# Performance work log

Measured on AMD Instinct MI355X. Metric: run time of the kernel, lower is better.

Reference implementation:

```python
import jax, jax.numpy as jnp
import numpy as np

D_MODEL = 3072
N_HEADS = 24
HEAD_DIM = D_MODEL // N_HEADS          # 128
Q_PROJ = D_MODEL // 2                  # 1536
KV_PROJ = 2 * D_MODEL // 3             # 2048
ROPE_DIM = HEAD_DIM // 2               # 64 (qk_rope_dim == qk_no_rope_dim)
MAX_LEN = 2048
ROPE_THETA = 10000.0
EPS = 1e-6
B, S = 2, 2048


def setup_inputs() -> dict:
    key = jax.random.key(0)
    ks = jax.random.split(key, 7)
    return {
        "x": jax.random.normal(ks[0], (B, S, D_MODEL), dtype=jnp.float32),
        "scale": jnp.ones((D_MODEL,), dtype=jnp.float32),
        "w_dq": 0.01 * jax.random.normal(ks[1], (D_MODEL, Q_PROJ), dtype=jnp.float32),
        "w_uq": 0.01 * jax.random.normal(ks[2], (Q_PROJ, D_MODEL), dtype=jnp.float32),
        "w_dkv": 0.01 * jax.random.normal(ks[3], (D_MODEL, KV_PROJ + ROPE_DIM), dtype=jnp.float32),
        "w_ukv": 0.01 * jax.random.normal(ks[4], (KV_PROJ, D_MODEL + N_HEADS * ROPE_DIM), dtype=jnp.float32),
        "w_o": 0.01 * jax.random.normal(ks[5], (D_MODEL, D_MODEL), dtype=jnp.float32),
    }


def _rope_cos_sin(seq_len):
    # freqs over full head_dim, sliced to rope_dim//2 then tiled x2 (as in torch repeat)
    freqs = 1.0 / (ROPE_THETA ** (jnp.arange(0, HEAD_DIM, 2, dtype=jnp.float32) / HEAD_DIM))
    angles = jnp.arange(seq_len, dtype=jnp.float32)[:, None] * freqs[None, :]  # [S, 64]
    ang = angles[:, : ROPE_DIM // 2]                                            # [S, 32]
    cos = jnp.tile(jnp.cos(ang), (1, 2))                                        # [S, 64]
    sin = jnp.tile(jnp.sin(ang), (1, 2))
    return cos[None, None], sin[None, None]  # [1,1,S,64]


def _rotate_half(t):
    a, b = jnp.split(t, 2, axis=-1)
    return jnp.concatenate([-b, a], axis=-1)


def reference(x, scale, w_dq, w_uq, w_dkv, w_ukv, w_o):
    b, s, _ = x.shape
    # RMSNorm pre-normalization
    xn = scale * (x * jax.lax.rsqrt(jnp.mean(x * x, axis=-1, keepdims=True) + EPS))
    # two-stage query projection
    q = (xn @ w_dq) @ w_uq                                   # [B,S,D]
    q = q.reshape(b, s, N_HEADS, HEAD_DIM).transpose(0, 2, 1, 3)  # [B,H,S,hd]
    q_no_rope, q_rope = jnp.split(q, [ROPE_DIM], axis=-1)
    cos, sin = _rope_cos_sin(s)
    q_rope = q_rope * cos + _rotate_half(q_rope) * sin
    # KV down projection (this is the kv cache)
    kv_down = xn @ w_dkv                                     # [B,S,KV_PROJ+rope]
    kv_no_rope, k_rope = jnp.split(kv_down, [KV_PROJ], axis=-1)
    # KV up projection
    kv_up = kv_no_rope @ w_ukv                               # [B,S,H*(hd+rope)]
    kv_up = kv_up.reshape(b, s, N_HEADS, HEAD_DIM + ROPE_DIM).transpose(0, 2, 1, 3)
    key, value = jnp.split(kv_up, [ROPE_DIM], axis=-1)       # key [B,H,S,64], value [B,H,S,128]
    # shared rope key (one head, broadcast to all heads)
    k_rope = k_rope[:, None, :, :]                           # [B,1,S,64]
    k_rope = k_rope * cos + _rotate_half(k_rope) * sin
    k_rope = jnp.broadcast_to(k_rope, (b, N_HEADS, s, ROPE_DIM))
    final_q = jnp.concatenate([q_no_rope, q_rope], axis=-1)  # [B,H,S,128]
    final_k = jnp.concatenate([key, k_rope], axis=-1)        # [B,H,S,128]
    # masked SDPA (causal, past_length=0)
    inv_scale = 1.0 / jnp.sqrt(jnp.asarray(HEAD_DIM, dtype=x.dtype))
    scores = jnp.einsum("bhsd,bhtd->bhst", final_q, final_k) * inv_scale
    causal = jnp.tril(jnp.ones((s, s), dtype=bool))
    scores = jnp.where(causal[None, None], scores, jnp.asarray(-1e30, dtype=scores.dtype))
    attn = jax.nn.softmax(scores, axis=-1)
    attn_out = jnp.einsum("bhst,bhtd->bhsd", attn, value)    # [B,H,S,128]
    attn_out = attn_out.transpose(0, 2, 1, 3).reshape(b, s, D_MODEL)
    output = attn_out @ w_o.T
    return output, kv_down
```

## Files before the change

kernel.cpp:

```cpp
#include <hip/hip_runtime.h>
#include <hip/hip_bf16.h>
#include <stdint.h>

using bf16_t = __bf16;
using bf16x8 = __attribute__((ext_vector_type(8))) __bf16;
using bf16x4 = __attribute__((ext_vector_type(4))) __bf16;
using f32x4  = __attribute__((ext_vector_type(4))) float;

#define D_MODEL 3072
#define N_HEADS 24
#define HEAD_DIM 128
#define Q_PROJ 1536
#define KV_PROJ 2048
#define ROPE_DIM 64
#define S_LEN 2048
#define NTOK 4096
#define KVDN 2112
#define KVUN 4608

__device__ __forceinline__ void async_ld16(const void* g, void* l) {
    __builtin_amdgcn_global_load_lds(
        (__attribute__((address_space(1))) uint32_t*)(uintptr_t)g,
        (__attribute__((address_space(3))) uint32_t*)(uint32_t)(uintptr_t)l,
        16, 0, 0);
}

#define BARRIER() __builtin_amdgcn_s_barrier()
#define WAITV4() asm volatile("s_waitcnt vmcnt(4)" ::: "memory")
#define WAITV0() asm volatile("s_waitcnt vmcnt(0)" ::: "memory")

__global__ __launch_bounds__(256) void rmsnorm_kernel(
    const float* __restrict__ x, const float* __restrict__ sc, bf16_t* __restrict__ xn)
{
    const int tok = blockIdx.x;
    const int t = threadIdx.x;
    const float4* xr = (const float4*)(x + (size_t)tok * D_MODEL);
    float4 a = xr[t], b = xr[t + 256], c = xr[t + 512];
    float ss = a.x*a.x + a.y*a.y + a.z*a.z + a.w*a.w
             + b.x*b.x + b.y*b.y + b.z*b.z + b.w*b.w
             + c.x*c.x + c.y*c.y + c.z*c.z + c.w*c.w;
    #pragma unroll
    for (int off = 32; off >= 1; off >>= 1) ss += __shfl_xor(ss, off);
    __shared__ float red[4];
    if ((t & 63) == 0) red[t >> 6] = ss;
    __syncthreads();
    const float inv = rsqrtf((red[0] + red[1] + red[2] + red[3]) * (1.0f / D_MODEL) + 1e-6f);
    const float4* sr = (const float4*)sc;
    float4 s0 = sr[t], s1 = sr[t + 256], s2 = sr[t + 512];
    bf16x4* xo = (bf16x4*)(xn + (size_t)tok * D_MODEL);
    bf16x4 o;
    o[0]=(bf16_t)(a.x*s0.x*inv); o[1]=(bf16_t)(a.y*s0.y*inv); o[2]=(bf16_t)(a.z*s0.z*inv); o[3]=(bf16_t)(a.w*s0.w*inv);
    xo[t] = o;
    o[0]=(bf16_t)(b.x*s1.x*inv); o[1]=(bf16_t)(b.y*s1.y*inv); o[2]=(bf16_t)(b.z*s1.z*inv); o[3]=(bf16_t)(b.w*s1.w*inv);
    xo[t + 256] = o;
    o[0]=(bf16_t)(c.x*s2.x*inv); o[1]=(bf16_t)(c.y*s2.y*inv); o[2]=(bf16_t)(c.z*s2.z*inv); o[3]=(bf16_t)(c.w*s2.w*inv);
    xo[t + 512] = o;
}

__global__ void transpose_conv(const float* __restrict__ in, bf16_t* __restrict__ out, int K, int N)
{
    __shared__ float tile[32][33];
    const int n0 = blockIdx.x * 32, k0 = blockIdx.y * 32;
    const int tx = threadIdx.x, ty = threadIdx.y;
    #pragma unroll
    for (int i = 0; i < 32; i += 8)
        tile[ty + i][tx] = in[(size_t)(k0 + ty + i) * N + n0 + tx];
    __syncthreads();
    #pragma unroll
    for (int i = 0; i < 32; i += 8)
        out[(size_t)(n0 + ty + i) * K + k0 + tx] = (bf16_t)tile[tx][ty + i];
}

__global__ void conv_bf16(const float* __restrict__ in, bf16_t* __restrict__ out, int n4)
{
    const int stride = gridDim.x * 256;
    for (int i = blockIdx.x * 256 + threadIdx.x; i < n4; i += stride) {
        float4 v = ((const float4*)in)[i];
        bf16x4 o;
        o[0] = (bf16_t)v.x; o[1] = (bf16_t)v.y; o[2] = (bf16_t)v.z; o[3] = (bf16_t)v.w;
        ((bf16x4*)out)[i] = o;
    }
}

template<int CFP>
__device__ __forceinline__ void mfma16(f32x4 (&acc)[8][4], const bf16x8 (&af)[8],
                                       const bf16x8 (&bfv)[2]) {
    __builtin_amdgcn_s_setprio(1);
    #pragma unroll
    for (int rf = 0; rf < 8; ++rf) {
        acc[rf][2*CFP]   = __builtin_amdgcn_mfma_f32_16x16x32_bf16(af[rf], bfv[0], acc[rf][2*CFP],   0, 0, 0);
        acc[rf][2*CFP+1] = __builtin_amdgcn_mfma_f32_16x16x32_bf16(af[rf], bfv[1], acc[rf][2*CFP+1], 0, 0, 0);
    }
    __builtin_amdgcn_s_setprio(0);
}

__global__ __launch_bounds__(512, 2) void gemm256(
    const bf16_t* __restrict__ A, const bf16_t* __restrict__ B, int N, int K,
    float* __restrict__ Cf, int ldf, int flo, int fhi,
    bf16_t* __restrict__ Cb1, int ldb1, int b1lo, int b1hi,
    bf16_t* __restrict__ Cb2, int ldb2, int b2lo, int b2hi)
{
    __shared__ char LDS[131072];
    char* Lc = LDS;
    const int tid = threadIdx.x;
    const int wv = tid >> 6, lane = tid & 63;
    const int fr = lane & 15, fg = lane >> 4;
    const int wr = wv >> 2, wc = wv & 3;
    const int m0 = blockIdx.y << 8, n0 = blockIdx.x << 8;
    const uint32_t slot4 = (uint32_t)((fg ^ ((fr >> 1) & 3)) << 4);

    int grow[2], gcol[2];
    const bf16_t* agp[2]; const bf16_t* bgp[2];
    uint32_t aoff[2], boff[2];
    #pragma unroll
    for (int j = 0; j < 2; ++j) {
        const int c = j * 512 + tid;
        const int g = c ^ ((c >> 3) & 3);
        grow[j] = g >> 2; gcol[j] = g & 3;
        agp[j] = A + (size_t)(m0 + grow[j]) * K + gcol[j] * 8;
        int br = n0 + grow[j]; if (br > N - 1) br = N - 1;
        bgp[j] = B + (size_t)br * K + gcol[j] * 8;
        aoff[j] = (uint32_t)((j * 8 + wv) * 1024);
        boff[j] = (uint32_t)(65536 + (j * 8 + wv) * 1024);
    }

    f32x4 acc[8][4];
    f32x4 zero = {0.f, 0.f, 0.f, 0.f};
    #pragma unroll
    for (int i = 0; i < 8; ++i)
        #pragma unroll
        for (int j = 0; j < 4; ++j) acc[i][j] = zero;

    bf16x8 af[8], bfv[2];
    const int rowA = (wr << 7) + fr;
    const int rowB = (wc << 6) + fr;

    auto stA = [&](int t, int kh) {
        const uint32_t sb = (uint32_t)(((2*t + kh) & 3) << 14);
        #pragma unroll
        for (int j = 0; j < 2; ++j)
            async_ld16(agp[j] + t * 64 + kh * 32, Lc + sb + aoff[j]);
    };
    auto stB = [&](int t, int kh) {
        const uint32_t sb = (uint32_t)(((2*t + kh) & 3) << 14);
        #pragma unroll
        for (int j = 0; j < 2; ++j)
            async_ld16(bgp[j] + t * 64 + kh * 32, Lc + sb + boff[j]);
    };
    auto ldA8 = [&](int t, int kh) {
        const uint32_t base = (uint32_t)(((2*t + kh) & 3) << 14);
        #pragma unroll
        for (int rf = 0; rf < 8; ++rf)
            af[rf] = *(const bf16x8*)(Lc + base + (rowA + rf * 16) * 64 + slot4);
    };
    auto ldB2 = [&](int t, int kh, int cfp) {
        const uint32_t base = (uint32_t)(65536 + (((2*t + kh) & 3) << 14));
        #pragma unroll
        for (int c = 0; c < 2; ++c)
            bfv[c] = *(const bf16x8*)(Lc + base + (rowB + (cfp * 2 + c) * 16) * 64 + slot4);
    };

    const int NT = K >> 6, nIter = NT >> 1;
    stA(0, 0); stB(0, 0); stA(0, 1); stB(0, 1); stA(1, 0); stB(1, 0);
    WAITV4(); BARRIER();

    for (int i = 0; i < nIter; ++i) {
        const int t0 = 2 * i, t1 = t0 + 1, t2 = t0 + 2, t3 = t0 + 3;
        const bool pref = (i < nIter - 1);
        ldA8(t0, 0); ldB2(t0, 0, 0); stA(t1, 1);
        BARRIER(); mfma16<0>(acc, af, bfv); BARRIER();
        ldB2(t0, 0, 1); stB(t1, 1);
        BARRIER(); mfma16<1>(acc, af, bfv); BARRIER();
        ldA8(t0, 1); ldB2(t0, 1, 0); if (pref) stA(t2, 0);
        BARRIER(); mfma16<0>(acc, af, bfv); BARRIER();
        ldB2(t0, 1, 1); if (pref) stB(t2, 0);
        if (pref) { WAITV4(); } else { WAITV0(); }
        BARRIER(); mfma16<1>(acc, af, bfv); BARRIER();
        ldA8(t1, 0); ldB2(t1, 0, 0); if (pref) stA(t2, 1);
        BARRIER(); mfma16<0>(acc, af, bfv); BARRIER();
        ldB2(t1, 0, 1); if (pref) stB(t2, 1);
        BARRIER(); mfma16<1>(acc, af, bfv); BARRIER();
        ldA8(t1, 1); ldB2(t1, 1, 0); if (pref) stA(t3, 0);
        BARRIER(); mfma16<0>(acc, af, bfv); BARRIER();
        ldB2(t1, 1, 1); if (pref) stB(t3, 0);
        WAITV4();
        BARRIER(); mfma16<1>(acc, af, bfv); BARRIER();
    }

    const int colb = n0 + (wc << 6) + fr;
    const int rowb = m0 + (wr << 7) + fg * 4;
    #pragma unroll
    for (int rf = 0; rf < 8; ++rf)
        #pragma unroll
        for (int cf = 0; cf < 4; ++cf) {
            const int col = colb + cf * 16;
            #pragma unroll
            for (int r = 0; r < 4; ++r) {
                const int row = rowb + rf * 16 + r;
                const float v = acc[rf][cf][r];
                if (Cf  && col >= flo  && col < fhi)  Cf [(size_t)row * ldf  + col - flo]  = v;
                if (Cb1 && col >= b1lo && col < b1hi) Cb1[(size_t)row * ldb1 + col - b1lo] = (bf16_t)v;
                if (Cb2 && col >= b2lo && col < b2hi) Cb2[(size_t)row * ldb2 + col - b2lo] = (bf16_t)v;
            }
        }
}

__global__ void rope_tab(float* __restrict__ ctab, float* __restrict__ stab)
{
    const int idx = blockIdx.x * 256 + threadIdx.x;
    if (idx >= S_LEN * 32) return;
    const int s = idx >> 5, i = idx & 31;
    const float freq = powf(10000.0f, -(float)(2 * i) * (1.0f / 128.0f));
    const float ang = (float)s * freq;
    ctab[idx] = cosf(ang);
    stab[idx] = sinf(ang);
}

__global__ void rope_q_kernel(bf16_t* __restrict__ q, const float* __restrict__ ctab,
                              const float* __restrict__ stab)
{
    const int idx = blockIdx.x * 256 + threadIdx.x;
    if (idx >= NTOK * N_HEADS * 32) return;
    const int i = idx & 31;
    const int rest = idx >> 5;
    const int h = rest % N_HEADS;
    const int tok = rest / N_HEADS;
    const int s = tok & (S_LEN - 1);
    bf16_t* p = q + (size_t)tok * D_MODEL + h * HEAD_DIM + 64;
    const float a = (float)p[i], b = (float)p[i + 32];
    const float c = ctab[s * 32 + i], sn = stab[s * 32 + i];
    p[i]      = (bf16_t)(a * c - b * sn);
    p[i + 32] = (bf16_t)(b * c + a * sn);
}

__global__ void rope_k_kernel(const float* __restrict__ kvd, bf16_t* __restrict__ kr,
                              const float* __restrict__ ctab, const float* __restrict__ stab)
{
    const int idx = blockIdx.x * 256 + threadIdx.x;
    if (idx >= NTOK * 32) return;
    const int i = idx & 31;
    const int tok = idx >> 5;
    const int s = tok & (S_LEN - 1);
    const float* p = kvd + (size_t)tok * KVDN + KV_PROJ;
    const float a = p[i], b = p[i + 32];
    const float c = ctab[s * 32 + i], sn = stab[s * 32 + i];
    kr[(size_t)tok * 64 + i]      = (bf16_t)(a * c - b * sn);
    kr[(size_t)tok * 64 + i + 32] = (bf16_t)(b * c + a * sn);
}

__global__ void vt_asm(const bf16_t* __restrict__ kvup, bf16_t* __restrict__ vt)
{
    __shared__ bf16_t tile[32][33];
    const int s0 = blockIdx.x * 32, d0 = blockIdx.y * 32, bh = blockIdx.z;
    const int b = bh / N_HEADS, h = bh % N_HEADS;
    const int tx = threadIdx.x, ty = threadIdx.y;
    #pragma unroll
    for (int i = 0; i < 32; i += 8)
        tile[ty + i][tx] = kvup[(size_t)(b * S_LEN + s0 + ty + i) * KVUN + h * 192 + 64 + d0 + tx];
    __syncthreads();
    #pragma unroll
    for (int i = 0; i < 32; i += 8)
        vt[((size_t)bh * HEAD_DIM + d0 + ty + i) * S_LEN + s0 + tx] = tile[tx][ty + i];
}

__global__ __launch_bounds__(256, 2) void attn_fwd(
    const bf16_t* __restrict__ Q, const bf16_t* __restrict__ KVUP,
    const bf16_t* __restrict__ KR, const bf16_t* __restrict__ VT,
    bf16_t* __restrict__ AO)
{
    __shared__ bf16_t Knr[2][64 * 64];
    __shared__ bf16_t Krp[2][64 * 64];
    __shared__ bf16_t Vls[2][128 * 64];

    const int bh = blockIdx.y;
    const int b = bh / N_HEADS, h = bh % N_HEADS;
    const int wave = threadIdx.x >> 6, lane = threadIdx.x & 63;
    const int fr = lane & 15, fg = lane >> 4;
    const int rx = fr & 7;
    const int hi = fg >> 1;
    const int s0l = fr + 32 * (fg & 1);
    const int s1l = s0l + 16;

    const bf16_t* Kb  = KVUP + (size_t)b * S_LEN * KVUN + (size_t)h * 192;
    const bf16_t* KRb = KR + (size_t)b * S_LEN * 64;
    const bf16_t* Vb  = VT + (size_t)bh * HEAD_DIM * S_LEN;

    const int srow   = lane >> 3;
    const int schunk = (lane & 7) ^ srow;
    const float l2e_isc = 0.127500625f;

    f32x4 zero = {0.f, 0.f, 0.f, 0.f};

    #pragma unroll 1
    for (int tp = 0; tp < 2; ++tp) {
        const int qt = (tp == 0) ? blockIdx.x : (15 - blockIdx.x);
        const int qb = qt * 128;
        const int wrow0 = qb + wave * 32;

        bf16x8 qf[2][4];
        #pragma unroll
        for (int rf = 0; rf < 2; ++rf)
            #pragma unroll
            for (int kc = 0; kc < 4; ++kc)
                qf[rf][kc] = *(const bf16x8*)(Q + (size_t)(b * S_LEN + wrow0 + rf * 16 + fr) * D_MODEL
                                              + h * HEAD_DIM + kc * 32 + fg * 8);
        f32x4 oacc[2][8];
        float m_i[2], l_i[2];
        #pragma unroll
        for (int rf = 0; rf < 2; ++rf) {
            #pragma unroll
            for (int nf = 0; nf < 8; ++nf) oacc[rf][nf] = zero;
            m_i[rf] = -1e30f; l_i[rf] = 0.f;
        }

        auto stage = [&](int kvb, int bf) {
            #pragma unroll
            for (int c = 0; c < 2; ++c) {
                const int r0 = wave * 16 + c * 8;
                async_ld16(Kb  + (size_t)(kvb + r0 + srow) * KVUN + schunk * 8, &Knr[bf][r0 * 64]);
                async_ld16(KRb + (size_t)(kvb + r0 + srow) * 64   + schunk * 8, &Krp[bf][r0 * 64]);
            }
            #pragma unroll
            for (int c = 0; c < 4; ++c) {
                const int r0 = wave * 32 + c * 8;
                async_ld16(Vb + (size_t)(r0 + srow) * S_LEN + kvb + schunk * 8, &Vls[bf][r0 * 64]);
            }
        };

        const int kvend = qb + 128;
        int cur = 0;
        stage(0, 0);
        __syncthreads();

        #pragma unroll 1
        for (int kvb = 0; kvb < kvend; kvb += 64) {
            if (kvb + 64 < kvend) stage(kvb + 64, cur ^ 1);

            if (kvb <= wrow0 + 31) {
                const bf16_t* Kc = Knr[cur];
                const bf16_t* Rc = Krp[cur];
                const bf16_t* Vc = Vls[cur];

                f32x4 sacc[2][4];
                #pragma unroll
                for (int rf = 0; rf < 2; ++rf)
                    #pragma unroll
                    for (int jn = 0; jn < 4; ++jn) sacc[rf][jn] = zero;
                #pragma unroll
                for (int jn = 0; jn < 4; ++jn) {
                    const int krow = jn * 16 + fr;
                    bf16x8 kA = *(const bf16x8*)(Kc + krow * 64 + (((0 + fg) ^ rx) << 3));
                    bf16x8 kB = *(const bf16x8*)(Kc + krow * 64 + (((4 + fg) ^ rx) << 3));
                    bf16x8 kC = *(const bf16x8*)(Rc + krow * 64 + (((0 + fg) ^ rx) << 3));
                    bf16x8 kD = *(const bf16x8*)(Rc + krow * 64 + (((4 + fg) ^ rx) << 3));
                    #pragma unroll
                    for (int rf = 0; rf < 2; ++rf) {
                        sacc[rf][jn] = __builtin_amdgcn_mfma_f32_16x16x32_bf16(kA, qf[rf][0], sacc[rf][jn], 0, 0, 0);
                        sacc[rf][jn] = __builtin_amdgcn_mfma_f32_16x16x32_bf16(kB, qf[rf][1], sacc[rf][jn], 0, 0, 0);
                        sacc[rf][jn] = __builtin_amdgcn_mfma_f32_16x16x32_bf16(kC, qf[rf][2], sacc[rf][jn], 0, 0, 0);
                        sacc[rf][jn] = __builtin_amdgcn_mfma_f32_16x16x32_bf16(kD, qf[rf][3], sacc[rf][jn], 0, 0, 0);
                    }
                }

                const bool needMask = (kvb + 63 > wrow0);
                uint32_t pk[2][4][2];
                float scf[2];
                #pragma unroll
                for (int rf = 0; rf < 2; ++rf) {
                    const int qrow = wrow0 + rf * 16 + fr;
                    float mx = -1e30f;
                    #pragma unroll
                    for (int jn = 0; jn < 4; ++jn)
                        #pragma unroll
                        for (int r = 0; r < 4; ++r) {
                            float v = sacc[rf][jn][r] * l2e_isc;
                            if (needMask && (kvb + jn * 16 + fg * 4 + r > qrow)) v = -1e30f;
                            sacc[rf][jn][r] = v;
                            mx = fmaxf(mx, v);
                        }
                    mx = fmaxf(mx, __shfl_xor(mx, 16));
                    mx = fmaxf(mx, __shfl_xor(mx, 32));
                    const float mn = fmaxf(m_i[rf], mx);
                    scf[rf] = __builtin_amdgcn_exp2f(m_i[rf] - mn);
                    m_i[rf] = mn;
                    float ls = 0.f;
                    #pragma unroll
                    for (int jn = 0; jn < 4; ++jn) {
                        float p0 = __builtin_amdgcn_exp2f(sacc[rf][jn][0] - mn);
                        float p1 = __builtin_amdgcn_exp2f(sacc[rf][jn][1] - mn);
                        float p2 = __builtin_amdgcn_exp2f(sacc[rf][jn][2] - mn);
                        float p3 = __builtin_amdgcn_exp2f(sacc[rf][jn][3] - mn);
                        ls += (p0 + p1) + (p2 + p3);
                        union { bf16x4 h; uint32_t w[2]; } cv;
                        cv.h[0] = (bf16_t)p0; cv.h[1] = (bf16_t)p1;
                        cv.h[2] = (bf16_t)p2; cv.h[3] = (bf16_t)p3;
                        pk[rf][jn][0] = cv.w[0]; pk[rf][jn][1] = cv.w[1];
                    }
                    ls += __shfl_xor(ls, 16);
                    ls += __shfl_xor(ls, 32);
                    l_i[rf] = l_i[rf] * scf[rf] + ls;
                    #pragma unroll
                    for (int nf = 0; nf < 8; ++nf)
                        #pragma unroll
                        for (int r = 0; r < 4; ++r) oacc[rf][nf][r] *= scf[rf];
                }

                bf16x8 bfr[2][2];
                #pragma unroll
                for (int rf = 0; rf < 2; ++rf)
                    #pragma unroll
                    for (int ks = 0; ks < 2; ++ks) {
                        const uint32_t t00 = __shfl(pk[rf][2*ks][0],   s0l);
                        const uint32_t t01 = __shfl(pk[rf][2*ks][1],   s0l);
                        const uint32_t t10 = __shfl(pk[rf][2*ks+1][0], s0l);
                        const uint32_t t11 = __shfl(pk[rf][2*ks+1][1], s0l);
                        const uint32_t u00 = __shfl(pk[rf][2*ks][0],   s1l);
                        const uint32_t u01 = __shfl(pk[rf][2*ks][1],   s1l);
                        const uint32_t u10 = __shfl(pk[rf][2*ks+1][0], s1l);
                        const uint32_t u11 = __shfl(pk[rf][2*ks+1][1], s1l);
                        union { bf16x8 h; uint32_t w[4]; } bb;
                        bb.w[0] = hi ? t10 : t00;
                        bb.w[1] = hi ? t11 : t01;
                        bb.w[2] = hi ? u10 : u00;
                        bb.w[3] = hi ? u11 : u01;
                        bfr[rf][ks] = bb.h;
                    }

                #pragma unroll
                for (int nf = 0; nf < 8; ++nf) {
                    const int vrow = nf * 16 + fr;
                    bf16x8 v0 = *(const bf16x8*)(Vc + vrow * 64 + (((0 + fg) ^ rx) << 3));
                    bf16x8 v1 = *(const bf16x8*)(Vc + vrow * 64 + (((4 + fg) ^ rx) << 3));
                    #pragma unroll
                    for (int rf = 0; rf < 2; ++rf) {
                        oacc[rf][nf] = __builtin_amdgcn_mfma_f32_16x16x32_bf16(v0, bfr[rf][0], oacc[rf][nf], 0, 0, 0);
                        oacc[rf][nf] = __builtin_amdgcn_mfma_f32_16x16x32_bf16(v1, bfr[rf][1], oacc[rf][nf], 0, 0, 0);
                    }
                }
            }
            __syncthreads();
            cur ^= 1;
        }

        #pragma unroll
        for (int rf = 0; rf < 2; ++rf) {
            const float rl = __builtin_amdgcn_rcpf(l_i[rf]);
            const int qrow = wrow0 + rf * 16 + fr;
            bf16_t* aob = AO + (size_t)(b * S_LEN + qrow) * D_MODEL + h * HEAD_DIM + fg * 4;
            #pragma unroll
            for (int nf = 0; nf < 8; ++nf) {
                bf16x4 o;
                o[0] = (bf16_t)(oacc[rf][nf][0] * rl);
                o[1] = (bf16_t)(oacc[rf][nf][1] * rl);
                o[2] = (bf16_t)(oacc[rf][nf][2] * rl);
                o[3] = (bf16_t)(oacc[rf][nf][3] * rl);
                *(bf16x4*)(aob + nf * 16) = o;
            }
        }
    }
}

extern "C" void kernel_launch(void* const* d_in, const int* in_sizes, int n_in,
                              void* d_out, int out_size, void* d_ws, size_t ws_size,
                              hipStream_t stream)
{
    const float* x     = (const float*)d_in[0];
    const float* scale = (const float*)d_in[1];
    const float* w_dq  = (const float*)d_in[2];
    const float* w_uq  = (const float*)d_in[3];
    const float* w_dkv = (const float*)d_in[4];
    const float* w_ukv = (const float*)d_in[5];
    const float* w_o   = (const float*)d_in[6];
    float* out0 = (float*)d_out;
    float* out1 = out0 + (size_t)NTOK * D_MODEL;

    if (ws_size < 187039744ull) return;
    char* ws = (char*)d_ws;
    bf16_t* XN    = (bf16_t*)(ws + 0);
    bf16_t* WCAT  = (bf16_t*)(ws + 25165824ull);
    bf16_t* WUQT  = (bf16_t*)(ws + 47579136ull);
    bf16_t* WUKVT = (bf16_t*)(ws + 57016320ull);
    bf16_t* WOB   = (bf16_t*)(ws + 75890688ull);
    bf16_t* QD    = (bf16_t*)(ws + 94765056ull);
    bf16_t* Qb    = (bf16_t*)(ws + 107347968ull);
    bf16_t* KVNR  = (bf16_t*)(ws + 132513792ull);
    bf16_t* KVUP  = (bf16_t*)(ws + 149291008ull);
    bf16_t* KRB   = (bf16_t*)(ws + 94765056ull);
    float*  CTAB  = (float*) (ws + 95289344ull);
    float*  STAB  = (float*) (ws + 95551488ull);
    bf16_t* VTb   = WCAT;
    bf16_t* AO    = XN;

    rmsnorm_kernel<<<NTOK, 256, 0, stream>>>(x, scale, XN);
    transpose_conv<<<dim3(1536/32, 3072/32), dim3(32,8), 0, stream>>>(w_dq,  WCAT, 3072, 1536);
    transpose_conv<<<dim3(2112/32, 3072/32), dim3(32,8), 0, stream>>>(w_dkv, WCAT + (size_t)1536*3072, 3072, 2112);
    transpose_conv<<<dim3(3072/32, 1536/32), dim3(32,8), 0, stream>>>(w_uq,  WUQT, 1536, 3072);
    transpose_conv<<<dim3(4608/32, 2048/32), dim3(32,8), 0, stream>>>(w_ukv, WUKVT, 2048, 4608);
    conv_bf16<<<2048, 256, 0, stream>>>(w_o, WOB, (D_MODEL * D_MODEL) / 4);

    gemm256<<<dim3(15, 16), 512, 0, stream>>>(XN, WCAT, 3648, 3072,
        out1, KVDN, 1536, 3648,
        QD,   Q_PROJ, 0, 1536,
        KVNR, KV_PROJ, 1536, 3584);
    gemm256<<<dim3(12, 16), 512, 0, stream>>>(QD, WUQT, 3072, 1536,
        nullptr, 0, 0, 0, Qb, D_MODEL, 0, 3072, nullptr, 0, 0, 0);
    rope_tab<<<(S_LEN * 32 + 255) / 256, 256, 0, stream>>>(CTAB, STAB);
    rope_q_kernel<<<(NTOK * N_HEADS * 32 + 255) / 256, 256, 0, stream>>>(Qb, CTAB, STAB);
    rope_k_kernel<<<(NTOK * 32 + 255) / 256, 256, 0, stream>>>(out1, KRB, CTAB, STAB);
    gemm256<<<dim3(18, 16), 512, 0, stream>>>(KVNR, WUKVT, 4608, 2048,
        nullptr, 0, 0, 0, KVUP, KVUN, 0, 4608, nullptr, 0, 0, 0);
    vt_asm<<<dim3(S_LEN/32, HEAD_DIM/32, 48), dim3(32,8), 0, stream>>>(KVUP, VTb);
    attn_fwd<<<dim3(8, 48), 256, 0, stream>>>(Qb, KVUP, KRB, VTb, AO);
    gemm256<<<dim3(12, 16), 512, 0, stream>>>(AO, WOB, 3072, 3072,
        out0, D_MODEL, 0, 3072, nullptr, 0, 0, 0, nullptr, 0, 0, 0);
}
```

Before: 555.2 us.

## Restructure GEMM main loop into row-half phases, swizzle block order, boost attention MFMA priority

The 256x256 GEMM inner loop now splits each 32-wide k-slice into two row-half phases. Each phase loads 4 A fragments and 4 B fragments and runs a 4x4 MFMA block, replacing the earlier 8x2 column-pair phases. An explicit lgkmcnt(0) wait plus sched_barrier is added before each MFMA phase, and the prefetch depth is shortened to one tile ahead. Workgroup IDs are remapped in groups of 8 to change which tiles run together on the GPU, and the attention kernel's QK and PV MFMA loops get s_setprio boosts. The intent is fewer LDS fragment reloads, better L2 locality and better MFMA issue, at the risk of less latency hiding from the shallower prefetch.

New measurement: 563.3 us. No clear change (+1.4%).

```diff
diff --git a/kernel.cpp b/kernel.cpp
--- a/kernel.cpp
+++ b/kernel.cpp
@@ -28,6 +28,8 @@
 #define BARRIER() __builtin_amdgcn_s_barrier()
 #define WAITV4() asm volatile("s_waitcnt vmcnt(4)" ::: "memory")
 #define WAITV0() asm volatile("s_waitcnt vmcnt(0)" ::: "memory")
+#define LGKM0()  do { asm volatile("s_waitcnt lgkmcnt(0)" ::: "memory"); \
+                      __builtin_amdgcn_sched_barrier(0); } while (0)
 
 __global__ __launch_bounds__(256) void rmsnorm_kernel(
     const float* __restrict__ x, const float* __restrict__ sc, bf16_t* __restrict__ xn)
@@ -82,15 +84,15 @@
     }
 }
 
-template<int CFP>
-__device__ __forceinline__ void mfma16(f32x4 (&acc)[8][4], const bf16x8 (&af)[8],
-                                       const bf16x8 (&bfv)[2]) {
+template<int RH>
+__device__ __forceinline__ void mfma16(f32x4 (&acc)[8][4], const bf16x8 (&af)[4],
+                                       const bf16x8 (&bfv)[4]) {
     __builtin_amdgcn_s_setprio(1);
     #pragma unroll
-    for (int rf = 0; rf < 8; ++rf) {
-        acc[rf][2*CFP]   = __builtin_amdgcn_mfma_f32_16x16x32_bf16(af[rf], bfv[0], acc[rf][2*CFP],   0, 0, 0);
-        acc[rf][2*CFP+1] = __builtin_amdgcn_mfma_f32_16x16x32_bf16(af[rf], bfv[1], acc[rf][2*CFP+1], 0, 0, 0);
-    }
+    for (int i = 0; i < 4; ++i)
+        #pragma unroll
+        for (int cf = 0; cf < 4; ++cf)
+            acc[RH*4+i][cf] = __builtin_amdgcn_mfma_f32_16x16x32_bf16(af[i], bfv[cf], acc[RH*4+i][cf], 0, 0, 0);
     __builtin_amdgcn_s_setprio(0);
 }
 
@@ -106,7 +108,13 @@
     const int wv = tid >> 6, lane = tid & 63;
     const int fr = lane & 15, fg = lane >> 4;
     const int wr = wv >> 2, wc = wv & 3;
-    const int m0 = blockIdx.y << 8, n0 = blockIdx.x << 8;
+
+    int lin = blockIdx.y * gridDim.x + blockIdx.x;
+    const int nwg = gridDim.x * gridDim.y;
+    if ((nwg & 7) == 0) lin = (lin & 7) * (nwg >> 3) + (lin >> 3);
+    const int bx = lin % gridDim.x, by = lin / gridDim.x;
+    const int m0 = by << 8, n0 = bx << 8;
+
     const uint32_t slot4 = (uint32_t)((fg ^ ((fr >> 1) & 3)) << 4);
 
     int grow[2], gcol[2];
@@ -131,7 +139,7 @@
         #pragma unroll
         for (int j = 0; j < 4; ++j) acc[i][j] = zero;
 
-    bf16x8 af[8], bfv[2];
+    bf16x8 af[4], bfv[4];
     const int rowA = (wr << 7) + fr;
     const int rowB = (wc << 6) + fr;
 
@@ -147,44 +155,43 @@
         for (int j = 0; j < 2; ++j)
             async_ld16(bgp[j] + t * 64 + kh * 32, Lc + sb + boff[j]);
     };
-    auto ldA8 = [&](int t, int kh) {
+    auto ldA4 = [&](int t, int kh, int rh) {
         const uint32_t base = (uint32_t)(((2*t + kh) & 3) << 14);
         #pragma unroll
-        for (int rf = 0; rf < 8; ++rf)
-            af[rf] = *(const bf16x8*)(Lc + base + (rowA + rf * 16) * 64 + slot4);
+        for (int i = 0; i < 4; ++i)
+            af[i] = *(const bf16x8*)(Lc + base + (rowA + (rh * 4 + i) * 16) * 64 + slot4);
     };
-    auto ldB2 = [&](int t, int kh, int cfp) {
+    auto ldB4 = [&](int t, int kh) {
         const uint32_t base = (uint32_t)(65536 + (((2*t + kh) & 3) << 14));
         #pragma unroll
-        for (int c = 0; c < 2; ++c)
-            bfv[c] = *(const bf16x8*)(Lc + base + (rowB + (cfp * 2 + c) * 16) * 64 + slot4);
+        for (int cf = 0; cf < 4; ++cf)
+            bfv[cf] = *(const bf16x8*)(Lc + base + (rowB + cf * 16) * 64 + slot4);
     };
 
-    const int NT = K >> 6, nIter = NT >> 1;
-    stA(0, 0); stB(0, 0); stA(0, 1); stB(0, 1); stA(1, 0); stB(1, 0);
+    const int NT = K >> 6;
+    stA(0, 0); stB(0, 0); stA(0, 1); stB(0, 1);
     WAITV4(); BARRIER();
 
-    for (int i = 0; i < nIter; ++i) {
-        const int t0 = 2 * i, t1 = t0 + 1, t2 = t0 + 2, t3 = t0 + 3;
-        const bool pref = (i < nIter - 1);
-        ldA8(t0, 0); ldB2(t0, 0, 0); stA(t1, 1);
-        BARRIER(); mfma16<0>(acc, af, bfv); BARRIER();
-        ldB2(t0, 0, 1); stB(t1, 1);
-        BARRIER(); mfma16<1>(acc, af, bfv); BARRIER();
-        ldA8(t0, 1); ldB2(t0, 1, 0); if (pref) stA(t2, 0);
-        BARRIER(); mfma16<0>(acc, af, bfv); BARRIER();
-        ldB2(t0, 1, 1); if (pref) stB(t2, 0);
+    for (int t = 0; t < NT; ++t) {
+        const bool pref = (t < NT - 1);
+        ldA4(t, 0, 0); ldB4(t, 0); if (pref) stA(t + 1, 0);
+        BARRIER(); LGKM0();
+        mfma16<0>(acc, af, bfv);
+        BARRIER();
+        ldA4(t, 0, 1); if (pref) stB(t + 1, 0);
         if (pref) { WAITV4(); } else { WAITV0(); }
-        BARRIER(); mfma16<1>(acc, af, bfv); BARRIER();
-        ldA8(t1, 0); ldB2(t1, 0, 0); if (pref) stA(t2, 1);
-        BARRIER(); mfma16<0>(acc, af, bfv); BARRIER();
-        ldB2(t1, 0, 1); if (pref) stB(t2, 1);
-        BARRIER(); mfma16<1>(acc, af, bfv); BARRIER();
-        ldA8(t1, 1); ldB2(t1, 1, 0); if (pref) stA(t3, 0);
-        BARRIER(); mfma16<0>(acc, af, bfv); BARRIER();
-        ldB2(t1, 1, 1); if (pref) stB(t3, 0);
+        BARRIER(); LGKM0();
+        mfma16<1>(acc, af, bfv);
+        BARRIER();
+        ldA4(t, 1, 0); ldB4(t, 1); if (pref) stA(t + 1, 1);
+        BARRIER(); LGKM0();
+        mfma16<0>(acc, af, bfv);
+        BARRIER();
+        ldA4(t, 1, 1); if (pref) stB(t + 1, 1);
         WAITV4();
-        BARRIER(); mfma16<1>(acc, af, bfv); BARRIER();
+        BARRIER(); LGKM0();
+        mfma16<1>(acc, af, bfv);
+        BARRIER();
     }
 
     const int colb = n0 + (wc << 6) + fr;
@@ -346,6 +353,7 @@
                 for (int rf = 0; rf < 2; ++rf)
                     #pragma unroll
                     for (int jn = 0; jn < 4; ++jn) sacc[rf][jn] = zero;
+                __builtin_amdgcn_s_setprio(1);
                 #pragma unroll
                 for (int jn = 0; jn < 4; ++jn) {
                     const int krow = jn * 16 + fr;
@@ -361,6 +369,7 @@
                         sacc[rf][jn] = __builtin_amdgcn_mfma_f32_16x16x32_bf16(kD, qf[rf][3], sacc[rf][jn], 0, 0, 0);
                     }
                 }
+                __builtin_amdgcn_s_setprio(0);
 
                 const bool needMask = (kvb + 63 > wrow0);
                 uint32_t pk[2][4][2];
@@ -426,6 +435,7 @@
                         bfr[rf][ks] = bb.h;
                     }
 
+                __builtin_amdgcn_s_setprio(1);
                 #pragma unroll
                 for (int nf = 0; nf < 8; ++nf) {
                     const int vrow = nf * 16 + fr;
@@ -437,6 +447,7 @@
                         oacc[rf][nf] = __builtin_amdgcn_mfma_f32_16x16x32_bf16(v1, bfr[rf][1], oacc[rf][nf], 0, 0, 0);
                     }
                 }
+                __builtin_amdgcn_s_setprio(0);
             }
             __syncthreads();
             cur ^= 1;
```
